# Optimization experiments

Hardware: AMD Instinct MI355X
Metric: run time of the kernel (lower is better)

Reference implementation:

```python
import jax, jax.numpy as jnp
import numpy as np

N_NODES = 100000
N_EDGES = 6400000
IN_CH, HID, OUT_CH = 14, 16, 8


def setup_inputs() -> dict:
    key = jax.random.key(0)
    ks = jax.random.split(key, 10)
    x = jax.random.normal(ks[0], (N_NODES, IN_CH), dtype=jnp.float32)
    edge_index = jax.random.randint(ks[1], (2, N_EDGES), 0, N_NODES, dtype=jnp.int64)
    edge_attr = jax.random.normal(ks[2], (N_EDGES, 4), dtype=jnp.float32)
    # SAGEConv params: lin_l (neighbor aggr, with bias), lin_r (root, no bias)
    def glorot(k, shape):
        fan_in = shape[1]
        return jax.random.normal(k, shape, dtype=jnp.float32) / jnp.sqrt(jnp.float32(fan_in))
    W1_l = glorot(ks[3], (HID, IN_CH)); b1 = jnp.zeros((HID,), jnp.float32)
    W1_r = glorot(ks[4], (HID, IN_CH))
    W2_l = glorot(ks[5], (OUT_CH, HID)); b2 = jnp.zeros((OUT_CH,), jnp.float32)
    W2_r = glorot(ks[6], (OUT_CH, HID))
    return {"x": x, "edge_index": edge_index, "edge_attr": edge_attr,
            "W1_l": W1_l, "b1": b1, "W1_r": W1_r,
            "W2_l": W2_l, "b2": b2, "W2_r": W2_r}


def sage_conv(x, src, dst, W_l, b_l, W_r):
    # mean aggregation of neighbor features at destination nodes
    msg = x[src]                                            # [E, F]
    s = jax.ops.segment_sum(msg, dst, num_segments=N_NODES)  # [N, F]
    cnt = jax.ops.segment_sum(jnp.ones((src.shape[0],), x.dtype), dst,
                              num_segments=N_NODES)
    mean = s / jnp.maximum(cnt, 1.0)[:, None]
    # out = lin_l(mean) + lin_r(x)
    return mean @ W_l.T + b_l + x @ W_r.T


def reference(x, edge_index, edge_attr, W1_l, b1, W1_r, W2_l, b2, W2_r):
    src, dst = edge_index[0], edge_index[1]
    h = jax.nn.relu(sage_conv(x, src, dst, W1_l, b1, W1_r))
    # F.dropout(training=self.training) -> identity in eval mode
    out = sage_conv(h, src, dst, W2_l, b2, W2_r)
    return out
```

## Files before the change

kernel.cpp:

```cpp
#include <hip/hip_runtime.h>

#define N_NODES 100000
#define N_EDGES 6400000
#define IN_CH 14
#define HID 16
#define OUT_CH 8

#define NBINS 1024
#define BINW 98
#define NCLS 8
#define SLABC 1152
#define BINREG (NCLS * SLABC)
#define BINBUF_WORDS (NBINS * BINREG)
#define SORT_CAP 7168
#define BF_THREADS 1024
#define BF_TILE 8192
#define BF_EPT (BF_TILE / BF_THREADS)
#define N_TILES ((N_EDGES + BF_TILE - 1) / BF_TILE)
#define LHN 128


__device__ __forceinline__ unsigned short f2bf(float f) {
    unsigned u = __float_as_uint(f);
    u += 0x7fffu + ((u >> 16) & 1u);
    return (unsigned short)(u >> 16);
}

__global__ void prep_kernel(const float* __restrict__ x, unsigned short* __restrict__ xb,
                            int* __restrict__ tail) {
    int i = blockIdx.x * blockDim.x + threadIdx.x;
    if (i < NCLS * NBINS) tail[i] = 0;
    if (i >= (NBINS * BINW) * 16) return;
    int n = i >> 4, c = i & 15;
    float v = (n < N_NODES && c < IN_CH) ? x[n * IN_CH + c] : 0.0f;
    xb[i] = f2bf(v);
}

__global__ __launch_bounds__(BF_THREADS)
void binfill_kernel(const uint4* __restrict__ src4, const uint4* __restrict__ dst4,
                    int* __restrict__ tail, unsigned* __restrict__ binbuf) {
    __shared__ unsigned stile[BF_TILE];
    __shared__ unsigned short stbin[BF_TILE];
    __shared__ int lh[NBINS];
    __shared__ int lx[NBINS];
    __shared__ int lofs[NBINS];
    __shared__ int wsum[16];

    const int t = threadIdx.x;
    const int lane = t & 63;
    const int wv = t >> 6;
    const int cls = blockIdx.x & (NCLS - 1);
    const long long tb = (long long)blockIdx.x * BF_TILE;

    lh[t] = 0;
    __syncthreads();

    unsigned epack[BF_EPT];
    int      ebin[BF_EPT];
    int      erank[BF_EPT];

#pragma unroll
    for (int sw = 0; sw < BF_EPT / 4; ++sw) {
        long long u = tb / 4 + (long long)sw * BF_THREADS + t;
        int k = sw * 4;
        if (u * 4 < N_EDGES) {
            uint4 s = src4[u];
            uint4 d = dst4[u];
            unsigned b;
            b = d.x / BINW; epack[k+0] = s.x | ((d.x - b*BINW) << 17); ebin[k+0] = (int)b; erank[k+0] = atomicAdd(&lh[b], 1);
            b = d.y / BINW; epack[k+1] = s.y | ((d.y - b*BINW) << 17); ebin[k+1] = (int)b; erank[k+1] = atomicAdd(&lh[b], 1);
            b = d.z / BINW; epack[k+2] = s.z | ((d.z - b*BINW) << 17); ebin[k+2] = (int)b; erank[k+2] = atomicAdd(&lh[b], 1);
            b = d.w / BINW; epack[k+3] = s.w | ((d.w - b*BINW) << 17); ebin[k+3] = (int)b; erank[k+3] = atomicAdd(&lh[b], 1);
        } else {
            ebin[k+0] = ebin[k+1] = ebin[k+2] = ebin[k+3] = -1;
        }
    }
    __syncthreads();

    int v = lh[t];
    int incl = v;
#pragma unroll
    for (int d = 1; d < 64; d <<= 1) {
        int o = __shfl_up(incl, d, 64);
        if (lane >= d) incl += o;
    }
    if (lane == 63) wsum[wv] = incl;
    __syncthreads();
    if (t < 16) {
        int s = wsum[t];
        int si = s;
#pragma unroll
        for (int d = 1; d < 16; d <<= 1) {
            int o = __shfl_up(si, d, 16);
            if (t >= d) si += o;
        }
        wsum[t] = si - s;
    }
    __syncthreads();
    lx[t] = incl - v + wsum[wv];
    lofs[t] = atomicAdd(&tail[cls * NBINS + t], v);
    __syncthreads();

#pragma unroll
    for (int k = 0; k < BF_EPT; ++k) {
        if (ebin[k] >= 0) {
            int pos = lx[ebin[k]] + erank[k];
            stile[pos] = epack[k];
            stbin[pos] = (unsigned short)ebin[k];
        }
    }
    __syncthreads();

    int cnt = (int)((N_EDGES - tb < BF_TILE) ? (N_EDGES - tb) : BF_TILE);
    for (int i = t; i < cnt; i += BF_THREADS) {
        int b = stbin[i];
        int slot = lofs[b] + (i - lx[b]);
        if ((unsigned)slot < (unsigned)SLABC)
            binbuf[b * BINREG + cls * SLABC + slot] = stile[i];
    }
}

__global__ __launch_bounds__(512)
void sortagg1_kernel(const unsigned* __restrict__ xb, const float* __restrict__ x,
                     unsigned* __restrict__ binbuf, const int* __restrict__ tail,
                     int* __restrict__ rowptr, int* __restrict__ deg,
                     const float* __restrict__ W_l, const float* __restrict__ bias,
                     const float* __restrict__ W_r,
                     float* __restrict__ h_f32, unsigned short* __restrict__ h_bf16) {
    __shared__ unsigned sbuf[SORT_CAP];
    __shared__ int lhist[LHN];
    __shared__ int loff[LHN];
    __shared__ int lcur[LHN];
    __shared__ int wtot[2];
    __shared__ int segcnt[NCLS];
    __shared__ int segoff[NCLS];
    __shared__ int totc[1];

    const int b = blockIdx.x;
    const int t = threadIdx.x;
    const int regbase = b * BINREG;

    if (t == 0) {
        int s = 0;
        for (int k = 0; k < NCLS; ++k) {
            int c = tail[k * NBINS + b];
            if (c < 0) c = 0;
            if (c > SLABC) c = SLABC;
            if (s + c > SORT_CAP) c = SORT_CAP - s;
            segcnt[k] = c; segoff[k] = s; s += c;
        }
        totc[0] = s;
    }
    if (t < LHN) lhist[t] = 0;
    __syncthreads();
    const int cnt = totc[0];

    for (int k = 0; k < NCLS; ++k) {
        const int base = regbase + k * SLABC;
        const int c = segcnt[k];
        for (int i = t; i < c; i += 512)
            atomicAdd(&lhist[binbuf[base + i] >> 17], 1);
    }
    __syncthreads();

    int v = (t < LHN) ? lhist[t] : 0;
    int incl = v;
#pragma unroll
    for (int d = 1; d < 64; d <<= 1) {
        int o = __shfl_up(incl, d, 64);
        if ((t & 63) >= d) incl += o;
    }
    if (t < LHN && (t & 63) == 63) wtot[t >> 6] = incl;
    __syncthreads();
    if (t < LHN) {
        int excl = incl - v + ((t >= 64) ? wtot[0] : 0);
        loff[t] = excl;
        lcur[t] = excl;
        if (t < BINW) {
            int gn = b * BINW + t;
            if (gn < N_NODES) { rowptr[gn] = regbase + excl; deg[gn] = v; }
        }
    }
    __syncthreads();

    for (int k = 0; k < NCLS; ++k) {
        const int base = regbase + k * SLABC;
        const int c = segcnt[k];
        for (int i = t; i < c; i += 512) {
            unsigned w = binbuf[base + i];
            unsigned ld = w >> 17;
            int pos = atomicAdd(&lcur[ld], 1);
            if (pos < cnt) sbuf[pos] = w & 0x1FFFFu;
        }
    }
    __syncthreads();

    for (int i = t; i < cnt; i += 512)
        binbuf[regbase + i] = sbuf[i];

    const int g = t >> 3;
    const int l = t & 7;
    float m0[2], m1[2];
#pragma unroll
    for (int p = 0; p < 2; ++p) {
        m0[p] = 0.0f; m1[p] = 0.0f;
        int n = g + 64 * p;
        if (n < BINW) {
            int dg = lhist[n];
            int off = loff[n];
            float a0 = 0.0f, a1 = 0.0f;
            int i = 0;
            for (; i + 4 <= dg; i += 4) {
                unsigned s0 = sbuf[off + i], s1 = sbuf[off + i + 1];
                unsigned s2 = sbuf[off + i + 2], s3 = sbuf[off + i + 3];
                unsigned u0 = xb[s0 * 8 + l];
                unsigned u1 = xb[s1 * 8 + l];
                unsigned u2 = xb[s2 * 8 + l];
                unsigned u3 = xb[s3 * 8 + l];
                a0 += __uint_as_float(u0 << 16);  a1 += __uint_as_float(u0 & 0xffff0000u);
                a0 += __uint_as_float(u1 << 16);  a1 += __uint_as_float(u1 & 0xffff0000u);
                a0 += __uint_as_float(u2 << 16);  a1 += __uint_as_float(u2 & 0xffff0000u);
                a0 += __uint_as_float(u3 << 16);  a1 += __uint_as_float(u3 & 0xffff0000u);
            }
            for (; i < dg; ++i) {
                unsigned u0 = xb[sbuf[off + i] * 8 + l];
                a0 += __uint_as_float(u0 << 16);  a1 += __uint_as_float(u0 & 0xffff0000u);
            }
            float inv = 1.0f / fmaxf((float)dg, 1.0f);
            m0[p] = a0 * inv; m1[p] = a1 * inv;
        }
    }
    __syncthreads();

    float* smean = (float*)sbuf;
#pragma unroll
    for (int p = 0; p < 2; ++p) {
        int n = g + 64 * p;
        if (n < BINW) {
            smean[n * 16 + 2 * l]     = m0[p];
            smean[n * 16 + 2 * l + 1] = m1[p];
        }
    }
    __syncthreads();

    const int nodeBase = b * BINW;
    for (int i = t; i < BINW * HID; i += 512) {
        int n = i >> 4, oc = i & 15;
        int gn = nodeBase + n;
        if (gn >= N_NODES) break;
        float a = bias[oc];
#pragma unroll
        for (int k = 0; k < IN_CH; ++k)
            a = fmaf(smean[n * 16 + k], W_l[oc * IN_CH + k],
                     fmaf(x[gn * IN_CH + k], W_r[oc * IN_CH + k], a));
        float vv = fmaxf(a, 0.0f);
        h_f32[gn * HID + oc] = vv;
        h_bf16[gn * HID + oc] = f2bf(vv);
    }
}

__global__ __launch_bounds__(512)
void agg2_kernel(const unsigned* __restrict__ hb,
                 const float* __restrict__ h_f32,
                 const unsigned* __restrict__ csr,
                 const int* __restrict__ rowptr, const int* __restrict__ deg,
                 const float* __restrict__ W_l, const float* __restrict__ bias,
                 const float* __restrict__ W_r, float* __restrict__ out) {
    __shared__ __attribute__((aligned(16))) unsigned sbuf[SORT_CAP];
    __shared__ int ldeg[LHN];
    __shared__ int loff[LHN];
    __shared__ int totc[1];

    const int b = blockIdx.x;
    const int t = threadIdx.x;
    const int regbase = b * BINREG;
    const int nvalid = (N_NODES - b * BINW < BINW) ? (N_NODES - b * BINW) : BINW;

    if (t < LHN) {
        int gn = b * BINW + t;
        int dv = 0, ov = 0;
        if (t < BINW && gn < N_NODES) {
            dv = deg[gn];
            ov = rowptr[gn] - regbase;
            if (dv < 0) dv = 0;
            if (ov < 0) ov = 0;
        }
        ldeg[t] = dv;
        loff[t] = ov;
    }
    if (t == 0) {
        int last = nvalid - 1;
        int c = (last >= 0) ? (rowptr[b * BINW + last] - regbase + deg[b * BINW + last]) : 0;
        if (c < 0) c = 0;
        if (c > SORT_CAP) c = SORT_CAP;
        totc[0] = c;
    }
    __syncthreads();
    const int cnt = totc[0];

    {
        const uint4* c4 = (const uint4*)(csr + regbase);
        uint4* s4 = (uint4*)sbuf;
        const int nv = cnt >> 2;
        for (int i = t; i < nv; i += 512) s4[i] = c4[i];
        int r = (nv << 2) + t;
        if (r < cnt) sbuf[r] = csr[regbase + r];
    }
    __syncthreads();

    const int g = t >> 3;
    const int l = t & 7;
    float m0[2], m1[2];
#pragma unroll
    for (int p = 0; p < 2; ++p) {
        m0[p] = 0.0f; m1[p] = 0.0f;
        int n = g + 64 * p;
        if (n < BINW) {
            int dg = ldeg[n];
            int off = loff[n];
            if (off + dg > cnt) dg = (cnt > off) ? (cnt - off) : 0;
            float a0 = 0.0f, a1 = 0.0f;
            int i = 0;
            for (; i + 4 <= dg; i += 4) {
                unsigned s0 = sbuf[off + i]     & 0x1FFFFu;
                unsigned s1 = sbuf[off + i + 1] & 0x1FFFFu;
                unsigned s2 = sbuf[off + i + 2] & 0x1FFFFu;
                unsigned s3 = sbuf[off + i + 3] & 0x1FFFFu;
                unsigned u0 = hb[s0 * 8 + l];
                unsigned u1 = hb[s1 * 8 + l];
                unsigned u2 = hb[s2 * 8 + l];
                unsigned u3 = hb[s3 * 8 + l];
                a0 += __uint_as_float(u0 << 16);  a1 += __uint_as_float(u0 & 0xffff0000u);
                a0 += __uint_as_float(u1 << 16);  a1 += __uint_as_float(u1 & 0xffff0000u);
                a0 += __uint_as_float(u2 << 16);  a1 += __uint_as_float(u2 & 0xffff0000u);
                a0 += __uint_as_float(u3 << 16);  a1 += __uint_as_float(u3 & 0xffff0000u);
            }
            for (; i < dg; ++i) {
                unsigned u0 = hb[(sbuf[off + i] & 0x1FFFFu) * 8 + l];
                a0 += __uint_as_float(u0 << 16);  a1 += __uint_as_float(u0 & 0xffff0000u);
            }
            float inv = 1.0f / fmaxf((float)dg, 1.0f);
            m0[p] = a0 * inv; m1[p] = a1 * inv;
        }
    }
    __syncthreads();

    float* smean = (float*)sbuf;
#pragma unroll
    for (int p = 0; p < 2; ++p) {
        int n = g + 64 * p;
        if (n < BINW) {
            smean[n * 16 + 2 * l]     = m0[p];
            smean[n * 16 + 2 * l + 1] = m1[p];
        }
    }
    __syncthreads();

    const int nodeBase = b * BINW;
    for (int i = t; i < BINW * OUT_CH; i += 512) {
        int n = i >> 3, oc = i & 7;
        int gn = nodeBase + n;
        if (gn >= N_NODES) break;
        float a = bias[oc];
#pragma unroll
        for (int k = 0; k < HID; ++k)
            a = fmaf(smean[n * 16 + k], W_l[oc * HID + k],
                     fmaf(h_f32[gn * HID + k], W_r[oc * HID + k], a));
        out[gn * OUT_CH + oc] = a;
    }
}

extern "C" void kernel_launch(void* const* d_in, const int* in_sizes, int n_in,
                              void* d_out, int out_size, void* d_ws, size_t ws_size,
                              hipStream_t stream) {
    const float* x    = (const float*)d_in[0];
    const int* eidx   = (const int*)d_in[1];
    const float* W1_l = (const float*)d_in[3];
    const float* b1   = (const float*)d_in[4];
    const float* W1_r = (const float*)d_in[5];
    const float* W2_l = (const float*)d_in[6];
    const float* b2   = (const float*)d_in[7];
    const float* W2_r = (const float*)d_in[8];
    float* out = (float*)d_out;

    const uint4* src4 = (const uint4*)eidx;
    const uint4* dst4 = (const uint4*)(eidx + N_EDGES);

    int*            wsi      = (int*)d_ws;
    unsigned*       binbuf   = (unsigned*)wsi;
    int*            tail     = wsi + 9437184;
    unsigned short* x_bf16   = (unsigned short*)(wsi + 9445376);
    unsigned short* h_bf16   = (unsigned short*)(wsi + 10248192);
    float*          h_f32    = (float*)(wsi + 11048192);
    int*            rowptr   = wsi + 12648192;
    int*            deg      = wsi + 12748544;

    prep_kernel<<<(NBINS * BINW * 16 + 1023) / 1024, 1024, 0, stream>>>(x, x_bf16, tail);
    binfill_kernel<<<N_TILES, BF_THREADS, 0, stream>>>(src4, dst4, tail, binbuf);
    sortagg1_kernel<<<NBINS, 512, 0, stream>>>((const unsigned*)x_bf16, x, binbuf, tail,
                                               rowptr, deg, W1_l, b1, W1_r, h_f32, h_bf16);
    agg2_kernel<<<NBINS, 512, 0, stream>>>((const unsigned*)h_bf16, h_f32, binbuf,
                                           rowptr, deg, W2_l, b2, W2_r, out);
}
```

Measured before the change: 286.9 us.

## Fuse both SAGE aggregation layers into one persistent kernel with grid barrier

Merges the first-layer sort/aggregate kernel and the second-layer aggregate kernel into a single kernel that keeps the per-bin sorted source list in shared memory. A software grid-wide barrier (an atomic counter reset in prep) separates layer one from layer two. This removes the write-back of the sorted CSR to global memory, the rowptr/deg arrays, and a second reload of the edge list. The barrier needs all 1024 blocks to be resident at once, which launch_bounds(512,8) is meant to allow. If they are not all co-resident it deadlocks, and spinning blocks add some latency.

```diff
diff --git a/kernel.cpp b/kernel.cpp
--- a/kernel.cpp
+++ b/kernel.cpp
@@ -27,8 +27,9 @@
 }
 
 __global__ void prep_kernel(const float* __restrict__ x, unsigned short* __restrict__ xb,
-                            int* __restrict__ tail) {
+                            int* __restrict__ tail, int* __restrict__ bar) {
     int i = blockIdx.x * blockDim.x + threadIdx.x;
+    if (i == 0) *bar = 0;
     if (i < NCLS * NBINS) tail[i] = 0;
     if (i >= (NBINS * BINW) * 16) return;
     int n = i >> 4, c = i & 15;
@@ -120,38 +121,46 @@
     }
 }
 
-__global__ __launch_bounds__(512)
-void sortagg1_kernel(const unsigned* __restrict__ xb, const float* __restrict__ x,
-                     unsigned* __restrict__ binbuf, const int* __restrict__ tail,
-                     int* __restrict__ rowptr, int* __restrict__ deg,
-                     const float* __restrict__ W_l, const float* __restrict__ bias,
-                     const float* __restrict__ W_r,
-                     float* __restrict__ h_f32, unsigned short* __restrict__ h_bf16) {
+__global__ __launch_bounds__(512, 8)
+void fusedagg_kernel(const unsigned* __restrict__ xb, const float* __restrict__ x,
+                     const unsigned* __restrict__ binbuf, const int* __restrict__ tail,
+                     const float* __restrict__ W1_l, const float* __restrict__ b1,
+                     const float* __restrict__ W1_r,
+                     float* __restrict__ h_f32, unsigned short* __restrict__ h_bf16,
+                     const float* __restrict__ W2_l, const float* __restrict__ b2,
+                     const float* __restrict__ W2_r, float* __restrict__ out,
+                     int* __restrict__ bar) {
     __shared__ unsigned sbuf[SORT_CAP];
+    __shared__ float smean[BINW * 16];
     __shared__ int lhist[LHN];
     __shared__ int loff[LHN];
     __shared__ int lcur[LHN];
     __shared__ int wtot[2];
     __shared__ int segcnt[NCLS];
-    __shared__ int segoff[NCLS];
     __shared__ int totc[1];
 
     const int b = blockIdx.x;
     const int t = threadIdx.x;
     const int regbase = b * BINREG;
-
+    const int g = t >> 3;
+    const int l = t & 7;
+
+    if (t < NCLS) {
+        int c = tail[t * NBINS + b];
+        if (c < 0) c = 0;
+        if (c > SLABC) c = SLABC;
+        segcnt[t] = c;
+    }
+    if (t < LHN) lhist[t] = 0;
     if (t == 0) {
         int s = 0;
         for (int k = 0; k < NCLS; ++k) {
-            int c = tail[k * NBINS + b];
-            if (c < 0) c = 0;
-            if (c > SLABC) c = SLABC;
-            if (s + c > SORT_CAP) c = SORT_CAP - s;
-            segcnt[k] = c; segoff[k] = s; s += c;
+            int c = segcnt[k];
+            if (s + c > SORT_CAP) { c = SORT_CAP - s; segcnt[k] = c; }
+            s += c;
         }
         totc[0] = s;
     }
-    if (t < LHN) lhist[t] = 0;
     __syncthreads();
     const int cnt = totc[0];
 
@@ -176,10 +185,6 @@
         int excl = incl - v + ((t >= 64) ? wtot[0] : 0);
         loff[t] = excl;
         lcur[t] = excl;
-        if (t < BINW) {
-            int gn = b * BINW + t;
-            if (gn < N_NODES) { rowptr[gn] = regbase + excl; deg[gn] = v; }
-        }
     }
     __syncthreads();
 
@@ -195,11 +200,6 @@
     }
     __syncthreads();
 
-    for (int i = t; i < cnt; i += 512)
-        binbuf[regbase + i] = sbuf[i];
-
-    const int g = t >> 3;
-    const int l = t & 7;
     float m0[2], m1[2];
 #pragma unroll
     for (int p = 0; p < 2; ++p) {
@@ -230,9 +230,6 @@
             m0[p] = a0 * inv; m1[p] = a1 * inv;
         }
     }
-    __syncthreads();
-
-    float* smean = (float*)sbuf;
 #pragma unroll
     for (int p = 0; p < 2; ++p) {
         int n = g + 64 * p;
@@ -248,84 +245,39 @@
         int n = i >> 4, oc = i & 15;
         int gn = nodeBase + n;
         if (gn >= N_NODES) break;
-        float a = bias[oc];
+        float a = b1[oc];
 #pragma unroll
         for (int k = 0; k < IN_CH; ++k)
-            a = fmaf(smean[n * 16 + k], W_l[oc * IN_CH + k],
-                     fmaf(x[gn * IN_CH + k], W_r[oc * IN_CH + k], a));
+            a = fmaf(smean[n * 16 + k], W1_l[oc * IN_CH + k],
+                     fmaf(x[gn * IN_CH + k], W1_r[oc * IN_CH + k], a));
         float vv = fmaxf(a, 0.0f);
         h_f32[gn * HID + oc] = vv;
         h_bf16[gn * HID + oc] = f2bf(vv);
     }
-}
-
-__global__ __launch_bounds__(512)
-void agg2_kernel(const unsigned* __restrict__ hb,
-                 const float* __restrict__ h_f32,
-                 const unsigned* __restrict__ csr,
-                 const int* __restrict__ rowptr, const int* __restrict__ deg,
-                 const float* __restrict__ W_l, const float* __restrict__ bias,
-                 const float* __restrict__ W_r, float* __restrict__ out) {
-    __shared__ __attribute__((aligned(16))) unsigned sbuf[SORT_CAP];
-    __shared__ int ldeg[LHN];
-    __shared__ int loff[LHN];
-    __shared__ int totc[1];
-
-    const int b = blockIdx.x;
-    const int t = threadIdx.x;
-    const int regbase = b * BINREG;
-    const int nvalid = (N_NODES - b * BINW < BINW) ? (N_NODES - b * BINW) : BINW;
-
-    if (t < LHN) {
-        int gn = b * BINW + t;
-        int dv = 0, ov = 0;
-        if (t < BINW && gn < N_NODES) {
-            dv = deg[gn];
-            ov = rowptr[gn] - regbase;
-            if (dv < 0) dv = 0;
-            if (ov < 0) ov = 0;
-        }
-        ldeg[t] = dv;
-        loff[t] = ov;
-    }
+
+    __syncthreads();
+    __threadfence();
     if (t == 0) {
-        int last = nvalid - 1;
-        int c = (last >= 0) ? (rowptr[b * BINW + last] - regbase + deg[b * BINW + last]) : 0;
-        if (c < 0) c = 0;
-        if (c > SORT_CAP) c = SORT_CAP;
-        totc[0] = c;
-    }
-    __syncthreads();
-    const int cnt = totc[0];
-
-    {
-        const uint4* c4 = (const uint4*)(csr + regbase);
-        uint4* s4 = (uint4*)sbuf;
-        const int nv = cnt >> 2;
-        for (int i = t; i < nv; i += 512) s4[i] = c4[i];
-        int r = (nv << 2) + t;
-        if (r < cnt) sbuf[r] = csr[regbase + r];
-    }
-    __syncthreads();
-
-    const int g = t >> 3;
-    const int l = t & 7;
-    float m0[2], m1[2];
+        __hip_atomic_fetch_add(bar, 1, __ATOMIC_ACQ_REL, __HIP_MEMORY_SCOPE_AGENT);
+        while (__hip_atomic_load(bar, __ATOMIC_ACQUIRE, __HIP_MEMORY_SCOPE_AGENT) < NBINS)
+            __builtin_amdgcn_s_sleep(8);
+    }
+    __syncthreads();
+    __threadfence();
+
+    const unsigned* hb = (const unsigned*)h_bf16;
 #pragma unroll
     for (int p = 0; p < 2; ++p) {
         m0[p] = 0.0f; m1[p] = 0.0f;
         int n = g + 64 * p;
         if (n < BINW) {
-            int dg = ldeg[n];
+            int dg = lhist[n];
             int off = loff[n];
-            if (off + dg > cnt) dg = (cnt > off) ? (cnt - off) : 0;
             float a0 = 0.0f, a1 = 0.0f;
             int i = 0;
             for (; i + 4 <= dg; i += 4) {
-                unsigned s0 = sbuf[off + i]     & 0x1FFFFu;
-                unsigned s1 = sbuf[off + i + 1] & 0x1FFFFu;
-                unsigned s2 = sbuf[off + i + 2] & 0x1FFFFu;
-                unsigned s3 = sbuf[off + i + 3] & 0x1FFFFu;
+                unsigned s0 = sbuf[off + i], s1 = sbuf[off + i + 1];
+                unsigned s2 = sbuf[off + i + 2], s3 = sbuf[off + i + 3];
                 unsigned u0 = hb[s0 * 8 + l];
                 unsigned u1 = hb[s1 * 8 + l];
                 unsigned u2 = hb[s2 * 8 + l];
@@ -336,7 +288,7 @@
                 a0 += __uint_as_float(u3 << 16);  a1 += __uint_as_float(u3 & 0xffff0000u);
             }
             for (; i < dg; ++i) {
-                unsigned u0 = hb[(sbuf[off + i] & 0x1FFFFu) * 8 + l];
+                unsigned u0 = hb[sbuf[off + i] * 8 + l];
                 a0 += __uint_as_float(u0 << 16);  a1 += __uint_as_float(u0 & 0xffff0000u);
             }
             float inv = 1.0f / fmaxf((float)dg, 1.0f);
@@ -344,8 +296,6 @@
         }
     }
     __syncthreads();
-
-    float* smean = (float*)sbuf;
 #pragma unroll
     for (int p = 0; p < 2; ++p) {
         int n = g + 64 * p;
@@ -356,16 +306,15 @@
     }
     __syncthreads();
 
-    const int nodeBase = b * BINW;
     for (int i = t; i < BINW * OUT_CH; i += 512) {
         int n = i >> 3, oc = i & 7;
         int gn = nodeBase + n;
         if (gn >= N_NODES) break;
-        float a = bias[oc];
+        float a = b2[oc];
 #pragma unroll
         for (int k = 0; k < HID; ++k)
-            a = fmaf(smean[n * 16 + k], W_l[oc * HID + k],
-                     fmaf(h_f32[gn * HID + k], W_r[oc * HID + k], a));
+            a = fmaf(smean[n * 16 + k], W2_l[oc * HID + k],
+                     fmaf(h_f32[gn * HID + k], W2_r[oc * HID + k], a));
         out[gn * OUT_CH + oc] = a;
     }
 }
@@ -392,13 +341,11 @@
     unsigned short* x_bf16   = (unsigned short*)(wsi + 9445376);
     unsigned short* h_bf16   = (unsigned short*)(wsi + 10248192);
     float*          h_f32    = (float*)(wsi + 11048192);
-    int*            rowptr   = wsi + 12648192;
-    int*            deg      = wsi + 12748544;
-
-    prep_kernel<<<(NBINS * BINW * 16 + 1023) / 1024, 1024, 0, stream>>>(x, x_bf16, tail);
+    int*            bar      = wsi + 12648192;
+
+    prep_kernel<<<(NBINS * BINW * 16 + 1023) / 1024, 1024, 0, stream>>>(x, x_bf16, tail, bar);
     binfill_kernel<<<N_TILES, BF_THREADS, 0, stream>>>(src4, dst4, tail, binbuf);
-    sortagg1_kernel<<<NBINS, 512, 0, stream>>>((const unsigned*)x_bf16, x, binbuf, tail,
-                                               rowptr, deg, W1_l, b1, W1_r, h_f32, h_bf16);
-    agg2_kernel<<<NBINS, 512, 0, stream>>>((const unsigned*)h_bf16, h_f32, binbuf,
-                                           rowptr, deg, W2_l, b2, W2_r, out);
-}
+    fusedagg_kernel<<<NBINS, 512, 0, stream>>>((const unsigned*)x_bf16, x, binbuf, tail,
+                                               W1_l, b1, W1_r, h_f32, h_bf16,
+                                               W2_l, b2, W2_r, out, bar);
+}
```

Result: slower. 853.0 us (+197.3%).
